# Performance work log

Measured on AMD Instinct MI355X. Metric: run time of the kernel, lower is better.

Reference implementation:

```python
import jax, jax.numpy as jnp
import numpy as np

EMBED = 256; HEADS = 8; LEVELS = 4; POINTS = 4; DIM = EMBED // HEADS


def _bilinear_gather(vflat, H, W, px, py):
    """grid_sample(mode='bilinear', padding='zeros', align_corners=False).
    vflat: (bs, heads, H*W, d); px, py: (bs, heads, nq, P) pixel coords.
    Returns (bs, heads, nq, P, d).
    """
    x0 = jnp.floor(px); y0 = jnp.floor(py)
    x1 = x0 + 1.0;      y1 = y0 + 1.0
    wx1 = px - x0; wx0 = 1.0 - wx1
    wy1 = py - y0; wy0 = 1.0 - wy1

    def corner(ix, iy, w):
        valid = (ix >= 0) & (ix <= W - 1) & (iy >= 0) & (iy <= H - 1)
        idx = (jnp.clip(iy, 0, H - 1) * W + jnp.clip(ix, 0, W - 1)).astype(jnp.int32)
        b, h, nq, P = idx.shape
        g = jnp.take_along_axis(vflat, idx.reshape(b, h, nq * P)[..., None], axis=2)
        g = g.reshape(b, h, nq, P, -1)
        return g * (w * valid)[..., None]

    return (corner(x0, y0, wx0 * wy0) + corner(x1, y0, wx1 * wy0)
            + corner(x0, y1, wx0 * wy1) + corner(x1, y1, wx1 * wy1))


def _ms_deform_attn(value4, shapes, loc, attn):
    """value4 (bs,nv,heads,D); loc (bs,nq,heads,L,P,2) in [0,1];
    attn (bs,nq,heads,L,P). Returns (bs,nq,heads*D)."""
    bs, nq = loc.shape[0], loc.shape[1]
    grids = 2.0 * loc - 1.0
    attn_t = jnp.transpose(attn, (0, 2, 1, 3, 4))  # (bs,heads,nq,L,P)
    out = jnp.zeros((bs, HEADS, nq, DIM), value4.dtype)
    start = 0
    for lvl in range(LEVELS):
        H, W = int(shapes[lvl, 0]), int(shapes[lvl, 1])
        v = value4[:, start:start + H * W]                 # (bs,HW,heads,D)
        vflat = jnp.transpose(v, (0, 2, 1, 3))             # (bs,heads,HW,D)
        g = jnp.transpose(grids[:, :, :, lvl], (0, 2, 1, 3, 4))  # (bs,heads,nq,P,2)
        px = (g[..., 0] + 1.0) * (W * 0.5) - 0.5
        py = (g[..., 1] + 1.0) * (H * 0.5) - 0.5
        sampled = _bilinear_gather(vflat, H, W, px, py)    # (bs,heads,nq,P,D)
        out = out + jnp.einsum('bhqpd,bhqp->bhqd', sampled, attn_t[:, :, :, lvl])
        start += H * W
    return jnp.transpose(out, (0, 2, 1, 3)).reshape(bs, nq, HEADS * DIM)


def _forward(query, value, query_pos, reference_points, last_reference_offsets,
             shapes, Wv, bv, Wo, bo, Wa, ba, Wout, bout):
    identity = query
    q = query + query_pos
    bs, nq, _ = q.shape
    nv = value.shape[1]
    v = (value @ Wv + bv).reshape(bs, nv, HEADS, DIM)
    off = (q @ Wo + bo).reshape(bs, nq, HEADS, LEVELS, POINTS, 2)
    attn = jax.nn.softmax((q @ Wa + ba).reshape(bs, nq, HEADS, LEVELS * POINTS), axis=-1)
    attn = attn.reshape(bs, nq, HEADS, LEVELS, POINTS)
    wh = jnp.asarray(np.asarray(shapes)[:, ::-1].copy(), jnp.float32)  # (L,2) as (w,h)
    loc = (reference_points[:, :, None, :, None, :]
           + off / wh[None, None, None, :, None, :]
           + last_reference_offsets[:, :, :, None, None, :])  # flow-guided per-head shift
    out = _ms_deform_attn(v, shapes, loc, attn)
    return out @ Wout + bout + identity  # dropout is identity at eval


def setup_inputs() -> dict:
    key = jax.random.key(0)
    ks = jax.random.split(key, 10)
    bs, nq = 8, 1200
    shapes = np.array([[92, 160], [46, 80], [23, 40], [12, 20]], np.int64)
    nv = int((shapes[:, 0] * shapes[:, 1]).sum())
    f = jnp.float32
    return {
        "query": jax.random.normal(ks[0], (bs, nq, EMBED), f),
        "value": jax.random.normal(ks[1], (bs, nv, EMBED), f),
        "query_pos": jax.random.normal(ks[2], (bs, nq, EMBED), f),
        "reference_points": jax.random.uniform(ks[3], (bs, nq, LEVELS, 2), f),
        "last_reference_offsets": jax.random.normal(ks[4], (bs, nq, HEADS, 2), f) * 0.02,
        "spatial_shapes": shapes,
        "Wv": jax.random.normal(ks[5], (EMBED, EMBED), f) * 0.02,
        "bv": jnp.zeros((EMBED,), f),
        "Wo": jax.random.normal(ks[6], (EMBED, HEADS * LEVELS * POINTS * 2), f) * 0.02,
        "bo": jax.random.normal(ks[7], (HEADS * LEVELS * POINTS * 2,), f) * 0.02,
        "Wa": jax.random.normal(ks[8], (EMBED, HEADS * LEVELS * POINTS), f) * 0.02,
        "ba": jnp.zeros((HEADS * LEVELS * POINTS,), f),
        "Wout": jax.random.normal(ks[9], (EMBED, EMBED), f) * 0.02,
        "bout": jnp.zeros((EMBED,), f),
    }


def reference(query, value, query_pos, reference_points, last_reference_offsets,
              spatial_shapes, Wv, bv, Wo, bo, Wa, ba, Wout, bout):
    return _forward(query, value, query_pos, reference_points, last_reference_offsets,
                    spatial_shapes, Wv, bv, Wo, bo, Wa, ba, Wout, bout)
```

## Files before the change

kernel.cpp:

```cpp
#include <hip/hip_runtime.h>
#include <math.h>

#define BS 8
#define NQ 1200
#define NV 19560
#define EMB 256
#define TPB 306

typedef __bf16 bf16;
typedef bf16 bf16x8 __attribute__((ext_vector_type(8)));
typedef float f32x4 __attribute__((ext_vector_type(4)));
typedef float f32x16 __attribute__((ext_vector_type(16)));

static __device__ __forceinline__ bf16x8 cvt8(float4 a, float4 b) {
    bf16x8 r;
    r[0] = (bf16)a.x; r[1] = (bf16)a.y; r[2] = (bf16)a.z; r[3] = (bf16)a.w;
    r[4] = (bf16)b.x; r[5] = (bf16)b.y; r[6] = (bf16)b.z; r[7] = (bf16)b.w;
    return r;
}

static __device__ __forceinline__ void gl16(const void* g, void* l) {
    __builtin_amdgcn_global_load_lds(
        (const __attribute__((address_space(1))) void*)g,
        (__attribute__((address_space(3))) void*)l, 16, 0, 0);
}

__global__ __launch_bounds__(256) void prep_k(
    const float* __restrict__ Wv, const float* __restrict__ Wo,
    const float* __restrict__ Wa, const float* __restrict__ Wout,
    const float* __restrict__ query, const float* __restrict__ qpos,
    const float* __restrict__ bo, const float* __restrict__ ba,
    bf16* __restrict__ Wv_p, bf16* __restrict__ Wo_p,
    bf16* __restrict__ Wa_p, bf16* __restrict__ Wout_p,
    bf16* __restrict__ qsum, float* __restrict__ cb)
{
    int bid = blockIdx.x, tid = threadIdx.x;
    if (bid < 896) {
        const float* src; bf16* dst; int N, t0;
        if (bid < 256)      { src = Wv;   dst = Wv_p;   N = 256; t0 = bid * 256; }
        else if (bid < 512) { src = Wo;   dst = Wo_p;   N = 256; t0 = (bid - 256) * 256; }
        else if (bid < 640) { src = Wa;   dst = Wa_p;   N = 128; t0 = (bid - 512) * 256; }
        else                { src = Wout; dst = Wout_p; N = 256; t0 = (bid - 640) * 256; }
        int t = t0 + tid;
        int n = t >> 8, k = t & 255;
        dst[t] = (bf16)src[k * N + n];
    } else if (bid < 10496) {
        int t = (bid - 896) * 256 + tid;
        qsum[t] = (bf16)(query[t] + qpos[t]);
    } else {
        cb[tid] = bo[tid];
        if (tid < 128) cb[256 + tid] = ba[tid];
    }
}

__global__ __launch_bounds__(256, 1) void vgemm_k(
    const float* __restrict__ A, const bf16* __restrict__ Bp,
    const float* __restrict__ bias, bf16* __restrict__ outB, int Mtiles)
{
    __shared__ __align__(16) bf16  sB[256 * 256];
    __shared__ __align__(16) float sA[4 * 2 * 1024];
    const int tid = threadIdx.x;
    const int lane = tid & 63;
    const int w = tid >> 6;
    const int l16 = lane & 15;
    const int qd = lane >> 4;

#pragma unroll
    for (int i = 0; i < 32; ++i) {
        int s = i * 256 + tid;
        int r = s >> 5, p = s & 31, c = p ^ (r & 7);
        gl16(Bp + (size_t)r * 256 + c * 8, sB + ((size_t)i * 256 + w * 64) * 8);
    }

    float* sAw = sA + w * 2048;
    const int lr4 = lane >> 4, sl = lane & 15;
    int swz4[4];
#pragma unroll
    for (int i = 0; i < 4; ++i) {
        int lr = i * 4 + lr4;
        swz4[i] = (sl ^ (lr & 7)) * 4;
    }
    auto stageT = [&](int b_, int p0_, int kc, int buf) {
#pragma unroll
        for (int i = 0; i < 4; ++i) {
            int pix = p0_ + w * 16 + i * 4 + lr4;
            pix = min(pix, NV - 1);
            gl16(A + ((size_t)b_ * NV + pix) * 256 + swz4[i] + kc * 64,
                 sAw + buf * 1024 + i * 256);
        }
    };

    int t = blockIdx.x;
    int b = t / TPB, p0 = (t - b * TPB) * 64;
    stageT(b, p0, 0, 0);
    stageT(b, p0, 1, 1);

    float bb[16];
#pragma unroll
    for (int ct = 0; ct < 16; ++ct) bb[ct] = bias[ct * 16 + l16];

    __syncthreads();

    const int akey = l16 & 7;
    f32x4 acc[16];

    auto compute = [&](int kc, int buf) {
        const float* ar = sAw + buf * 1024 + l16 * 64;
#pragma unroll
        for (int ks = 0; ks < 2; ++ks) {
            int kg = kc * 2 + ks;
            int s  = ks * 8 + qd * 2;
            float4 a0 = *(const float4*)(ar + ((s    ) ^ akey) * 4);
            float4 a1 = *(const float4*)(ar + ((s + 1) ^ akey) * 4);
            bf16x8 af = cvt8(a0, a1);
#pragma unroll
            for (int ct = 0; ct < 16; ++ct) {
                int brow = ct * 16 + l16;
                bf16x8 bfr = *(const bf16x8*)(sB + (size_t)brow * 256 +
                                              ((kg * 4 + qd) ^ (brow & 7)) * 8);
                acc[ct] = __builtin_amdgcn_mfma_f32_16x16x32_bf16(af, bfr, acc[ct], 0, 0, 0);
            }
        }
    };

#define VM_WAIT4 asm volatile("s_waitcnt vmcnt(4)" ::: "memory")
#define VM_WAIT0 asm volatile("s_waitcnt vmcnt(0)" ::: "memory")

    while (true) {
#pragma unroll
        for (int ct = 0; ct < 16; ++ct) acc[ct] = (f32x4){0.f, 0.f, 0.f, 0.f};

        VM_WAIT4; compute(0, 0); stageT(b, p0, 2, 0);
        VM_WAIT4; compute(1, 1); stageT(b, p0, 3, 1);
        VM_WAIT4; compute(2, 0);
        VM_WAIT0; compute(3, 1);

#pragma unroll
        for (int ct = 0; ct < 16; ++ct) {
            const bf16* dst0 = outB + ((size_t)(b * 8 + (ct >> 1)) * NV) * 32 + (ct & 1) * 16 + l16;
#pragma unroll
            for (int r = 0; r < 4; ++r) {
                int pix = p0 + w * 16 + qd * 4 + r;
                if (pix < NV)
                    *(bf16*)(dst0 + (size_t)pix * 32) = (bf16)(acc[ct][r] + bb[ct]);
            }
        }

        int tn = t + gridDim.x;
        if (tn >= Mtiles) break;
        t = tn;
        b = t / TPB; p0 = (t - b * TPB) * 64;
        stageT(b, p0, 0, 0);
        stageT(b, p0, 1, 1);
    }
#undef VM_WAIT4
#undef VM_WAIT0
}

template <int NS, int NB, int NGRP, bool HAS_RES, bool OUT_BF16>
__global__ __launch_bounds__(256, 2) void gemm3_k(
    const bf16* __restrict__ Ah, const bf16* __restrict__ Bp,
    const float* __restrict__ bias, const float* __restrict__ res,
    float* __restrict__ outF, bf16* __restrict__ outB, int Mtiles)
{
    constexpr int CT = NB / 16;
    __shared__ __align__(16) bf16 sB[NB * 256];
    const int tid = threadIdx.x;
    const int lane = tid & 63;
    const int w = tid >> 6;
    const int l16 = lane & 15;
    const int qd = lane >> 4;
    const int col0 = (blockIdx.x % NGRP) * NB;
    const int tstride = gridDim.x / NGRP;
    const bf16* Bsrc = Bp + (size_t)col0 * 256;

    uint4 curH[8], nxtH[8];
    auto loadA = [&](int t, uint4* dH) {
        size_t rb = ((size_t)t * 64 + w * 16 + l16) * 256;
#pragma unroll
        for (int kc = 0; kc < 8; ++kc)
            dH[kc] = *(const uint4*)(Ah + rb + kc * 32 + qd * 8);
    };

    int tile = blockIdx.x / NGRP;
    if (tile < Mtiles) loadA(tile, curH);

#pragma unroll
    for (int i = 0; i < NB * 32 / 256; ++i) {
        int s = i * 256 + tid;
        int r = s >> 5, p = s & 31, c = p ^ (r & 7);
        gl16(Bsrc + (size_t)r * 256 + c * 8, sB + (size_t)(i * 256 + w * 64) * 8);
    }
    __syncthreads();

    for (; tile < Mtiles; tile += tstride) {
        int nt = tile + tstride;
        if (nt < Mtiles) loadA(nt, nxtH);

        f32x4 acc[CT];
#pragma unroll
        for (int c = 0; c < CT; ++c) acc[c] = (f32x4){0.f, 0.f, 0.f, 0.f};
#pragma unroll
        for (int kc = 0; kc < 8; ++kc) {
            bf16x8 af = *(const bf16x8*)&curH[kc];
#pragma unroll
            for (int ct = 0; ct < CT; ++ct) {
                int brow = ct * 16 + l16;
                int chunk = (kc * 4 + qd) ^ (l16 & 7);
                bf16x8 bfr = *(const bf16x8*)(sB + (size_t)brow * 256 + chunk * 8);
                acc[ct] = __builtin_amdgcn_mfma_f32_16x16x32_bf16(af, bfr, acc[ct], 0, 0, 0);
            }
        }
#pragma unroll
        for (int ct = 0; ct < CT; ++ct) {
            int col = col0 + ct * 16 + l16;
            float bbv = bias[col];
#pragma unroll
            for (int r = 0; r < 4; ++r) {
                int row = tile * 64 + w * 16 + qd * 4 + r;
                size_t idx = (size_t)row * NS + col;
                float v = acc[ct][r] + bbv;
                if (HAS_RES) v += res[(size_t)row * 256 + col];
                if (OUT_BF16) outB[idx] = (bf16)v;
                else          outF[idx] = v;
            }
        }
#pragma unroll
        for (int i = 0; i < 8; ++i) curH[i] = nxtH[i];
    }
}

static __device__ __forceinline__ void b8f(uint4 u, float* f) {
    f[0] = __uint_as_float(u.x << 16); f[1] = __uint_as_float(u.x & 0xffff0000u);
    f[2] = __uint_as_float(u.y << 16); f[3] = __uint_as_float(u.y & 0xffff0000u);
    f[4] = __uint_as_float(u.z << 16); f[5] = __uint_as_float(u.z & 0xffff0000u);
    f[6] = __uint_as_float(u.w << 16); f[7] = __uint_as_float(u.w & 0xffff0000u);
}

__global__ __launch_bounds__(256) void sample4_k(
    const bf16* __restrict__ vv, const float* __restrict__ comb,
    const float* __restrict__ refp, const float* __restrict__ lref,
    bf16* __restrict__ outb)
{
    const int cH[4] = {92, 46, 23, 12};
    const int cW[4] = {160, 80, 40, 20};
    const int cS[4] = {0, 14720, 18400, 19320};
    const int w = threadIdx.x >> 6;
    const int lane = threadIdx.x & 63;
    const int wid = blockIdx.x * 4 + w;
    const int bq = wid >> 3, h = wid & 7;
    const int b = bq / NQ;
    const int p = lane >> 2, dg = lane & 3;
    const int lvl = p >> 2;

    float logit = comb[(size_t)bq * 384 + 256 + h * 16 + p];
    float mx = logit;
#pragma unroll
    for (int s = 4; s < 64; s <<= 1) mx = fmaxf(mx, __shfl_xor(mx, s));
    float e = __expf(logit - mx);
    float ssum = e;
#pragma unroll
    for (int s = 4; s < 64; s <<= 1) ssum += __shfl_xor(ssum, s);
    float wgt = e / ssum;

    const int Hh = cH[lvl], Ww = cW[lvl];
    float ox = comb[(size_t)bq * 384 + h * 32 + p * 2];
    float oy = comb[(size_t)bq * 384 + h * 32 + p * 2 + 1];
    float rx = refp[(size_t)bq * 8 + lvl * 2];
    float ry = refp[(size_t)bq * 8 + lvl * 2 + 1];
    float lrx = lref[(size_t)bq * 16 + h * 2];
    float lry = lref[(size_t)bq * 16 + h * 2 + 1];

    float px = (rx + ox / (float)Ww + lrx) * (float)Ww - 0.5f;
    float py = (ry + oy / (float)Hh + lry) * (float)Hh - 0.5f;
    float x0f = floorf(px), y0f = floorf(py);
    int x0 = (int)x0f, y0 = (int)y0f;
    float wx1 = px - x0f, wx0 = 1.f - wx1;
    float wy1 = py - y0f, wy0 = 1.f - wy1;
    bool xa = (unsigned)x0 < (unsigned)Ww, xb = (unsigned)(x0 + 1) < (unsigned)Ww;
    bool ya = (unsigned)y0 < (unsigned)Hh, yb = (unsigned)(y0 + 1) < (unsigned)Hh;
    int xc0 = min(max(x0, 0), Ww - 1), xc1 = min(max(x0 + 1, 0), Ww - 1);
    int yc0 = min(max(y0, 0), Hh - 1), yc1 = min(max(y0 + 1, 0), Hh - 1);
    float w00 = wgt * wx0 * wy0 * (float)(xa && ya);
    float w01 = wgt * wx1 * wy0 * (float)(xb && ya);
    float w10 = wgt * wx0 * wy1 * (float)(xa && yb);
    float w11 = wgt * wx1 * wy1 * (float)(xb && yb);

    const bf16* vb = vv + ((size_t)(b * 8 + h) * NV + cS[lvl]) * 32 + dg * 8;
    uint4 g00 = *(const uint4*)(vb + ((size_t)yc0 * Ww + xc0) * 32);
    uint4 g01 = *(const uint4*)(vb + ((size_t)yc0 * Ww + xc1) * 32);
    uint4 g10 = *(const uint4*)(vb + ((size_t)yc1 * Ww + xc0) * 32);
    uint4 g11 = *(const uint4*)(vb + ((size_t)yc1 * Ww + xc1) * 32);

    float acc[8], f[8];
    b8f(g00, f);
#pragma unroll
    for (int j = 0; j < 8; j++) acc[j] = w00 * f[j];
    b8f(g01, f);
#pragma unroll
    for (int j = 0; j < 8; j++) acc[j] = fmaf(w01, f[j], acc[j]);
    b8f(g10, f);
#pragma unroll
    for (int j = 0; j < 8; j++) acc[j] = fmaf(w10, f[j], acc[j]);
    b8f(g11, f);
#pragma unroll
    for (int j = 0; j < 8; j++) acc[j] = fmaf(w11, f[j], acc[j]);

#pragma unroll
    for (int s = 4; s < 64; s <<= 1)
#pragma unroll
        for (int j = 0; j < 8; j++) acc[j] += __shfl_xor(acc[j], s);

    if (p == 0) {
        bf16x8 o;
#pragma unroll
        for (int j = 0; j < 8; j++) o[j] = (bf16)acc[j];
        *(bf16x8*)(outb + (size_t)bq * 256 + h * 32 + dg * 8) = o;
    }
}

extern "C" void kernel_launch(void* const* d_in, const int* in_sizes, int n_in,
                              void* d_out, int out_size, void* d_ws, size_t ws_size,
                              hipStream_t stream) {
    (void)in_sizes; (void)n_in; (void)out_size; (void)ws_size;
    const float* query = (const float*)d_in[0];
    const float* value = (const float*)d_in[1];
    const float* qpos  = (const float*)d_in[2];
    const float* refp  = (const float*)d_in[3];
    const float* lref  = (const float*)d_in[4];
    const float* Wv   = (const float*)d_in[6];
    const float* bv   = (const float*)d_in[7];
    const float* Wo   = (const float*)d_in[8];
    const float* bo   = (const float*)d_in[9];
    const float* Wa   = (const float*)d_in[10];
    const float* ba   = (const float*)d_in[11];
    const float* Wout = (const float*)d_in[12];
    const float* bout = (const float*)d_in[13];

    char* ws = (char*)d_ws;
    bf16*  Wv_p   = (bf16*)(ws + 0);
    bf16*  Wo_p   = (bf16*)(ws + 131072);
    bf16*  Wa_p   = (bf16*)(ws + 262144);
    bf16*  Wout_p = (bf16*)(ws + 327680);
    bf16*  qsum   = (bf16*)(ws + 458752);
    float* comb   = (float*)(ws + 5373952);
    bf16*  tsa_b  = (bf16*)(ws + 20119552);
    bf16*  v_b    = (bf16*)(ws + 25034752);
    float* cbias  = (float*)(ws + 105152512);

    prep_k<<<10497, 256, 0, stream>>>(Wv, Wo, Wa, Wout, query, qpos, bo, ba,
                                      Wv_p, Wo_p, Wa_p, Wout_p, qsum, cbias);

    vgemm_k<<<256, 256, 0, stream>>>(value, Wv_p, bv, v_b, BS * TPB);
    gemm3_k<384, 128, 3, false, false><<<450, 256, 0, stream>>>(
        qsum, Wo_p, cbias, nullptr, comb, nullptr, (BS * NQ) / 64);
    sample4_k<<<(BS * NQ * 8) / 4, 256, 0, stream>>>(v_b, comb, refp, lref, tsa_b);
    gemm3_k<256, 128, 2, true, false><<<300, 256, 0, stream>>>(
        tsa_b, Wout_p, bout, query, (float*)d_out, nullptr, (BS * NQ) / 64);
}
```

Baseline: 395.8 us.

## Double per-wave rows in value projection GEMM and prefetch next tile across iterations

The value-projection kernel now processes 128-pixel tiles, with each wave computing two 16-row MFMA blocks that share the same B fragment. Staging moves to 32-wide k chunks across 8 steps, and the first two chunks of the next tile are prefetched during the last compute steps, so tiles no longer wait on a fresh load. This halves B reads from LDS per output row and keeps loads in flight between tiles. The cost is double the accumulator registers (32 f32x4), which may lower occupancy. If Mtiles is not updated by the host for the new TPB, the tile count becomes wrong.

After: 396.5 us. About the same (+0.2%).

```diff
diff --git a/kernel.cpp b/kernel.cpp
--- a/kernel.cpp
+++ b/kernel.cpp
@@ -5,7 +5,7 @@
 #define NQ 1200
 #define NV 19560
 #define EMB 256
-#define TPB 306
+#define TPB 153
 
 typedef __bf16 bf16;
 typedef bf16 bf16x8 __attribute__((ext_vector_type(8)));
@@ -73,27 +73,21 @@
     }
 
     float* sAw = sA + w * 2048;
-    const int lr4 = lane >> 4, sl = lane & 15;
-    int swz4[4];
-#pragma unroll
-    for (int i = 0; i < 4; ++i) {
-        int lr = i * 4 + lr4;
-        swz4[i] = (sl ^ (lr & 7)) * 4;
-    }
-    auto stageT = [&](int b_, int p0_, int kc, int buf) {
+    const int arow = lane >> 3;
+    const int aslot = (lane & 7) ^ arow;
+    auto stageT = [&](int t_, int kg, int buf) {
+        int b_ = t_ / TPB, p0_ = (t_ - b_ * TPB) * 128;
 #pragma unroll
         for (int i = 0; i < 4; ++i) {
-            int pix = p0_ + w * 16 + i * 4 + lr4;
-            pix = min(pix, NV - 1);
-            gl16(A + ((size_t)b_ * NV + pix) * 256 + swz4[i] + kc * 64,
+            int pix = min(p0_ + w * 32 + i * 8 + arow, NV - 1);
+            gl16(A + ((size_t)b_ * NV + pix) * 256 + kg * 32 + aslot * 4,
                  sAw + buf * 1024 + i * 256);
         }
     };
 
     int t = blockIdx.x;
-    int b = t / TPB, p0 = (t - b * TPB) * 64;
-    stageT(b, p0, 0, 0);
-    stageT(b, p0, 1, 1);
+    stageT(t, 0, 0);
+    stageT(t, 1, 1);
 
     float bb[16];
 #pragma unroll
@@ -102,59 +96,68 @@
     __syncthreads();
 
     const int akey = l16 & 7;
-    f32x4 acc[16];
-
-    auto compute = [&](int kc, int buf) {
-        const float* ar = sAw + buf * 1024 + l16 * 64;
-#pragma unroll
-        for (int ks = 0; ks < 2; ++ks) {
-            int kg = kc * 2 + ks;
-            int s  = ks * 8 + qd * 2;
-            float4 a0 = *(const float4*)(ar + ((s    ) ^ akey) * 4);
-            float4 a1 = *(const float4*)(ar + ((s + 1) ^ akey) * 4);
-            bf16x8 af = cvt8(a0, a1);
-#pragma unroll
-            for (int ct = 0; ct < 16; ++ct) {
-                int brow = ct * 16 + l16;
-                bf16x8 bfr = *(const bf16x8*)(sB + (size_t)brow * 256 +
-                                              ((kg * 4 + qd) ^ (brow & 7)) * 8);
-                acc[ct] = __builtin_amdgcn_mfma_f32_16x16x32_bf16(af, bfr, acc[ct], 0, 0, 0);
-            }
+    f32x4 acc0[16], acc1[16];
+
+    auto compute = [&](int kg, int buf) {
+        const float* ab = sAw + buf * 1024;
+        const float* ar0 = ab + l16 * 32;
+        const float* ar1 = ab + (16 + l16) * 32;
+        float4 a00 = *(const float4*)(ar0 + ((qd * 2    ) ^ akey) * 4);
+        float4 a01 = *(const float4*)(ar0 + ((qd * 2 + 1) ^ akey) * 4);
+        float4 a10 = *(const float4*)(ar1 + ((qd * 2    ) ^ akey) * 4);
+        float4 a11 = *(const float4*)(ar1 + ((qd * 2 + 1) ^ akey) * 4);
+        bf16x8 af0 = cvt8(a00, a01);
+        bf16x8 af1 = cvt8(a10, a11);
+#pragma unroll
+        for (int ct = 0; ct < 16; ++ct) {
+            int brow = ct * 16 + l16;
+            bf16x8 bfr = *(const bf16x8*)(sB + (size_t)brow * 256 +
+                                          ((kg * 4 + qd) ^ (brow & 7)) * 8);
+            acc0[ct] = __builtin_amdgcn_mfma_f32_16x16x32_bf16(af0, bfr, acc0[ct], 0, 0, 0);
+            acc1[ct] = __builtin_amdgcn_mfma_f32_16x16x32_bf16(af1, bfr, acc1[ct], 0, 0, 0);
         }
     };
 
 #define VM_WAIT4 asm volatile("s_waitcnt vmcnt(4)" ::: "memory")
-#define VM_WAIT0 asm volatile("s_waitcnt vmcnt(0)" ::: "memory")
 
     while (true) {
 #pragma unroll
-        for (int ct = 0; ct < 16; ++ct) acc[ct] = (f32x4){0.f, 0.f, 0.f, 0.f};
-
-        VM_WAIT4; compute(0, 0); stageT(b, p0, 2, 0);
-        VM_WAIT4; compute(1, 1); stageT(b, p0, 3, 1);
-        VM_WAIT4; compute(2, 0);
-        VM_WAIT0; compute(3, 1);
-
+        for (int ct = 0; ct < 16; ++ct) {
+            acc0[ct] = (f32x4){0.f, 0.f, 0.f, 0.f};
+            acc1[ct] = (f32x4){0.f, 0.f, 0.f, 0.f};
+        }
+
+        int tn = t + gridDim.x;
+        const bool last = (tn >= Mtiles);
+
+        VM_WAIT4; compute(0, 0); stageT(t, 2, 0);
+        VM_WAIT4; compute(1, 1); stageT(t, 3, 1);
+        VM_WAIT4; compute(2, 0); stageT(t, 4, 0);
+        VM_WAIT4; compute(3, 1); stageT(t, 5, 1);
+        VM_WAIT4; compute(4, 0); stageT(t, 6, 0);
+        VM_WAIT4; compute(5, 1); stageT(t, 7, 1);
+        VM_WAIT4; compute(6, 0); if (!last) stageT(tn, 0, 0);
+        VM_WAIT4; compute(7, 1); if (!last) stageT(tn, 1, 1);
+
+        int b = t / TPB, p0 = (t - b * TPB) * 128;
 #pragma unroll
         for (int ct = 0; ct < 16; ++ct) {
             const bf16* dst0 = outB + ((size_t)(b * 8 + (ct >> 1)) * NV) * 32 + (ct & 1) * 16 + l16;
 #pragma unroll
             for (int r = 0; r < 4; ++r) {
-                int pix = p0 + w * 16 + qd * 4 + r;
-                if (pix < NV)
-                    *(bf16*)(dst0 + (size_t)pix * 32) = (bf16)(acc[ct][r] + bb[ct]);
+                int pix0 = p0 + w * 32 + qd * 4 + r;
+                if (pix0 < NV)
+                    *(bf16*)(dst0 + (size_t)pix0 * 32) = (bf16)(acc0[ct][r] + bb[ct]);
+                int pix1 = pix0 + 16;
+                if (pix1 < NV)
+                    *(bf16*)(dst0 + (size_t)pix1 * 32) = (bf16)(acc1[ct][r] + bb[ct]);
             }
         }
 
-        int tn = t + gridDim.x;
-        if (tn >= Mtiles) break;
+        if (last) break;
         t = tn;
-        b = t / TPB; p0 = (t - b * TPB) * 64;
-        stageT(b, p0, 0, 0);
-        stageT(b, p0, 1, 1);
     }
 #undef VM_WAIT4
-#undef VM_WAIT0
 }
 
 template <int NS, int NB, int NGRP, bool HAS_RES, bool OUT_BF16>
```
